# Performance work log

Measured on AMD Instinct MI355X. Metric: run time of the kernel, lower is better.

Reference implementation:

```python
import jax, jax.numpy as jnp
import numpy as np

EPS = 1e-8  # torch CosineSimilarity default eps


def setup_inputs() -> dict:
    key = jax.random.key(0)
    k1, k2, k3, k4 = jax.random.split(key, 4)
    cur_insts = jax.random.randint(k1, (200, 1024), 0, 50000)          # [S, B] token ids
    W = jax.random.normal(k2, (50000, 300), dtype=jnp.float32)          # embedding table
    train_embs = jax.random.normal(k3, (100000, 300), dtype=jnp.float32)  # pooled train embeddings
    y_train = jax.random.randint(k4, (100000,), 0, 1000)                # train labels
    return {"cur_insts": cur_insts, "W": W, "train_embs": train_embs, "y_train": y_train}


def reference(cur_insts, W, train_embs, y_train):
    # Embed + mean-pool over the sequence axis (dim 0 in the torch code)
    x = W[cur_insts].mean(axis=0)                                   # [B, d]
    # Cosine similarity: x.y / (max(||x||,eps) * max(||y||,eps))
    xn = jnp.maximum(jnp.linalg.norm(x, axis=1, keepdims=True), EPS)        # [B, 1]
    tn = jnp.maximum(jnp.linalg.norm(train_embs, axis=1, keepdims=True), EPS)  # [N, 1]
    sims = (x @ train_embs.T) / (xn * tn.T)                         # [B, N]
    nn_idx = jnp.argmax(sims, axis=1)                               # [B]
    scores = jnp.max(sims, axis=1)                                  # [B]
    y_pred = y_train[nn_idx]                                        # [B]
    return y_pred, scores
```

## Files before the change

### kernel.cpp

```cpp
#include <hip/hip_runtime.h>
#include <hip/hip_bf16.h>
#include <stdint.h>

#define EPS 1e-8f

typedef __attribute__((ext_vector_type(8))) short bf16x8;
typedef __attribute__((ext_vector_type(4))) float f32x4;
typedef unsigned long long u64;
typedef unsigned int u32;

constexpr int SEQ = 200;
constexpr int B_  = 1024;
constexpr int D_  = 300;
constexpr int DP  = 320;
constexpr int NT  = 100000;
constexpr int BM = 128, BN = 128, BK = 64;
constexpr int NSTRIP = 784;
constexpr int NTP = NSTRIP * BN;
constexpr int CAND_MAX = 4096;
#define MARGIN 2e-3f

__device__ __forceinline__ unsigned short f2bf(float f) {
    u32 b = __float_as_uint(f);
    return (unsigned short)((b + 0x7fffu + ((b >> 16) & 1u)) >> 16);
}
__device__ __forceinline__ u32 simkey(float s) {
    u32 b = __float_as_uint(s);
    return (b & 0x80000000u) ? ~b : (b | 0x80000000u);
}
__device__ __forceinline__ float keysim(u32 k) {
    u32 b = (k & 0x80000000u) ? (k & 0x7fffffffu) : ~k;
    return __uint_as_float(b);
}
__device__ __forceinline__ void gload_lds16(const void* g, void* l) {
    __builtin_amdgcn_global_load_lds(
        (const __attribute__((address_space(1))) unsigned int*)g,
        (__attribute__((address_space(3))) unsigned int*)l, 16, 0, 0);
}

__global__ __launch_bounds__(640) void pool_kernel(
    const int* __restrict__ ids, const float* __restrict__ W,
    float* __restrict__ x, unsigned short* __restrict__ xh,
    float* __restrict__ rxn)
{
    const int b = blockIdx.x;
    const int tid = threadIdx.x;
    __shared__ int sid[SEQ];
    __shared__ float part[640];
    for (int s = tid; s < SEQ; s += 640) sid[s] = ids[s * B_ + b];
    __syncthreads();
    const int half = (tid >= 320) ? 1 : 0;
    const int d = tid - half * 320;
    float a0 = 0.f, a1 = 0.f;
    if (d < D_) {
        const int s0 = half * (SEQ / 2);
        #pragma unroll 2
        for (int s = 0; s < SEQ / 2; s += 2) {
            a0 += W[(size_t)sid[s0 + s]     * D_ + d];
            a1 += W[(size_t)sid[s0 + s + 1] * D_ + d];
        }
    }
    part[tid] = a0 + a1;
    __syncthreads();
    float xv = 0.f;
    if (tid < 320) xv = (part[tid] + part[tid + 320]) * (1.0f / SEQ);
    __syncthreads();
    if (tid < 320) part[tid] = (tid < D_) ? xv * xv : 0.f;
    __syncthreads();
    if (tid < 64) {
        float s = 0.f;
        #pragma unroll
        for (int i = 0; i < 5; ++i) s += part[tid + i * 64];
        #pragma unroll
        for (int m = 32; m >= 1; m >>= 1) s += __shfl_xor(s, m, 64);
        if (tid == 0) rxn[b] = 1.0f / fmaxf(sqrtf(s), EPS);
    }
    if (tid < 320) {
        if (tid < D_) {
            x[(size_t)b * D_ + tid] = xv;
            xh[(size_t)b * DP + tid] = f2bf(xv);
        } else {
            xh[(size_t)b * DP + tid] = 0;
        }
    }
}

__global__ __launch_bounds__(256) void tnorm_kernel(
    const float* __restrict__ T, float* __restrict__ rtn,
    unsigned short* __restrict__ Tb)
{
    const int n = blockIdx.x * 4 + (threadIdx.x >> 6);
    const int lane = threadIdx.x & 63;
    if (n >= NTP) return;
    ushort4* tb = (ushort4*)(Tb + (size_t)n * DP);
    if (n >= NT) {
        ushort4 z = {0, 0, 0, 0};
        tb[lane] = z;
        if (lane < 16) tb[64 + lane] = z;
        return;
    }
    const float4* Tr = (const float4*)(T + (size_t)n * D_);
    float4 v = Tr[lane];
    float s = v.x * v.x + v.y * v.y + v.z * v.z + v.w * v.w;
    ushort4 o; o.x = f2bf(v.x); o.y = f2bf(v.y); o.z = f2bf(v.z); o.w = f2bf(v.w);
    tb[lane] = o;
    if (lane < 16) {
        if (lane < 11) {
            float4 w = Tr[64 + lane];
            s += w.x * w.x + w.y * w.y + w.z * w.z + w.w * w.w;
            ushort4 p; p.x = f2bf(w.x); p.y = f2bf(w.y); p.z = f2bf(w.z); p.w = f2bf(w.w);
            tb[64 + lane] = p;
        } else {
            ushort4 z = {0, 0, 0, 0};
            tb[64 + lane] = z;
        }
    }
    #pragma unroll
    for (int m = 32; m >= 1; m >>= 1) s += __shfl_xor(s, m, 64);
    if (lane == 0) rtn[n] = 1.0f / fmaxf(sqrtf(s), EPS);
}

__global__ __launch_bounds__(256, 3) void gemm_hh_kernel(
    const unsigned short* __restrict__ Ah, const unsigned short* __restrict__ Tb,
    const float* __restrict__ rxn, const float* __restrict__ rtn,
    u32* __restrict__ blockmax)
{
    __shared__ unsigned short sA[BM * BK];
    __shared__ unsigned short sB[BN * BK];
    __shared__ u32 sBest[BM];

    const int tid = threadIdx.x;
    const int g = blockIdx.x;
    const int k8 = g & 7;
    const int t = g >> 3;
    const int bMi = t & 7;
    const int strip = ((t >> 3) << 3) | k8;

    const int lane = tid & 63, wid = tid >> 6;
    const int wm = wid >> 1, wn = wid & 1;
    const int quad = lane >> 4, l15 = lane & 15;

    const unsigned short* pA[4];
    const unsigned short* pB[4];
    int ldsoff[4];
    #pragma unroll
    for (int j = 0; j < 4; ++j) {
        int L = (j * 4 + wid) * 64 + lane;
        int r = L >> 3;
        int c = (L & 7) ^ (r & 7);
        ldsoff[j] = (j * 4 + wid) * 1024;
        pA[j] = Ah + (size_t)(bMi * BM + r) * DP + c * 8;
        pB[j] = Tb + (size_t)(strip * BN + r) * DP + c * 8;
    }

    f32x4 acc[4][4] = {};

    for (int kp = 0; kp < DP; kp += BK) {
        #pragma unroll
        for (int j = 0; j < 4; ++j)
            gload_lds16(pA[j] + kp, (char*)sA + ldsoff[j]);
        #pragma unroll
        for (int j = 0; j < 4; ++j)
            gload_lds16(pB[j] + kp, (char*)sB + ldsoff[j]);
        __syncthreads();

        #pragma unroll
        for (int s = 0; s < 2; ++s) {
            bf16x8 fa[4], fb[4];
            #pragma unroll
            for (int f = 0; f < 4; ++f) {
                int ar = wm * 64 + f * 16 + l15;
                int ac = (s * 4 + quad) ^ (ar & 7);
                fa[f] = *(const bf16x8*)&sA[ar * BK + ac * 8];
                int br = wn * 64 + f * 16 + l15;
                int bc = (s * 4 + quad) ^ (br & 7);
                fb[f] = *(const bf16x8*)&sB[br * BK + bc * 8];
            }
            #pragma unroll
            for (int fm = 0; fm < 4; ++fm)
                #pragma unroll
                for (int fn = 0; fn < 4; ++fn)
                    acc[fm][fn] = __builtin_amdgcn_mfma_f32_16x16x32_bf16(
                        fa[fm], fb[fn], acc[fm][fn], 0, 0, 0);
        }
        __syncthreads();
    }

    if (tid < BM) sBest[tid] = 0u;
    __syncthreads();
    float rt[4];
    const int gn0 = strip * BN + wn * 64 + l15;
    #pragma unroll
    for (int fn = 0; fn < 4; ++fn)
        rt[fn] = (gn0 + fn * 16 < NT) ? rtn[gn0 + fn * 16] : 0.f;
    #pragma unroll
    for (int fm = 0; fm < 4; ++fm) {
        #pragma unroll
        for (int r = 0; r < 4; ++r) {
            int rowl = wm * 64 + fm * 16 + quad * 4 + r;
            float rx = rxn[bMi * BM + rowl];
            u32 bk = 0u;
            #pragma unroll
            for (int fn = 0; fn < 4; ++fn) {
                float sim = acc[fm][fn][r] * rx * rt[fn];
                u32 k = simkey(sim);
                bk = (k > bk) ? k : bk;
            }
            #pragma unroll
            for (int m = 1; m < 16; m <<= 1) {
                u32 o = __shfl_xor(bk, m, 64);
                bk = (o > bk) ? o : bk;
            }
            if (l15 == 0) atomicMax(&sBest[rowl], bk);
        }
    }
    __syncthreads();
    if (tid < BM)
        blockmax[(size_t)(bMi * BM + tid) * NSTRIP + strip] = sBest[tid];
}

__global__ __launch_bounds__(256) void scan_kernel(
    const u32* __restrict__ blockmax, u32* __restrict__ cand,
    u32* __restrict__ count)
{
    const int row = blockIdx.x;
    const int t = threadIdx.x;
    const u32* bmr = blockmax + (size_t)row * NSTRIP;
    u32 m = 0u;
    for (int j = t; j < NSTRIP; j += 256) { u32 e = bmr[j]; m = (e > m) ? e : m; }
    #pragma unroll
    for (int msk = 32; msk >= 1; msk >>= 1) {
        u32 o = __shfl_xor(m, msk, 64);
        m = (o > m) ? o : m;
    }
    __shared__ u32 wred[4];
    __shared__ float thr_s;
    if ((t & 63) == 0) wred[t >> 6] = m;
    __syncthreads();
    if (t == 0) {
        u32 gmx = wred[0];
        for (int i = 1; i < 4; ++i) gmx = (wred[i] > gmx) ? wred[i] : gmx;
        thr_s = keysim(gmx) - MARGIN;
    }
    __syncthreads();
    float thr = thr_s;
    for (int j = t; j < NSTRIP; j += 256) {
        if (keysim(bmr[j]) >= thr) {
            u32 p = atomicAdd(count, 1u);
            if (p < CAND_MAX) cand[p] = ((u32)row << 10) | (u32)j;
        }
    }
}

__global__ __launch_bounds__(256) void rescore_kernel(
    const u32* __restrict__ cand, const u32* __restrict__ count,
    const float* __restrict__ x, const float* __restrict__ T,
    const float* __restrict__ rxn, u64* __restrict__ winner)
{
    u32 cnt = *count; if (cnt > CAND_MAX) cnt = CAND_MAX;
    if (blockIdx.x >= cnt) return;
    u32 c = cand[blockIdx.x];
    const int row = c >> 10, strip = c & 1023;
    __shared__ float4 xs4[75];
    const int t = threadIdx.x;
    if (t < 75) xs4[t] = *(const float4*)&x[(size_t)row * D_ + t * 4];
    __syncthreads();
    const float rx = rxn[row];
    const int w = t >> 6, lane = t & 63;
    u64 best = 0ull;
    for (int cc = 0; cc < 32; ++cc) {
        int n = strip * BN + w * 32 + cc;
        if (n >= NT) break;
        const float4* Tr = (const float4*)(T + (size_t)n * D_);
        float4 v = Tr[lane], xv = xs4[lane];
        float dot = v.x * xv.x + v.y * xv.y + v.z * xv.z + v.w * xv.w;
        float tt  = v.x * v.x + v.y * v.y + v.z * v.z + v.w * v.w;
        if (lane < 11) {
            float4 v2 = Tr[lane + 64], x2 = xs4[lane + 64];
            dot += v2.x * x2.x + v2.y * x2.y + v2.z * x2.z + v2.w * x2.w;
            tt  += v2.x * v2.x + v2.y * v2.y + v2.z * v2.z + v2.w * v2.w;
        }
        #pragma unroll
        for (int m = 32; m >= 1; m >>= 1) {
            dot += __shfl_xor(dot, m, 64);
            tt  += __shfl_xor(tt, m, 64);
        }
        float sim = dot * rx / fmaxf(sqrtf(tt), EPS);
        u64 pk = ((u64)simkey(sim) << 32) | (u32)(~n);
        best = (pk > best) ? pk : best;
    }
    if (lane == 0 && best) atomicMax(&winner[row], best);
}

__global__ __launch_bounds__(64) void final_kernel(
    const u64* __restrict__ winner, const float* __restrict__ x,
    const float* __restrict__ T, const int* __restrict__ y_train,
    float* __restrict__ out)
{
    const int b = blockIdx.x;
    const int lane = threadIdx.x;
    int idx = (int)(~(u32)winner[b]);
    if (idx < 0 || idx >= NT) idx = 0;
    double dot = 0.0, nx = 0.0, nt = 0.0;
    for (int d = lane; d < D_; d += 64) {
        double xv = (double)x[(size_t)b * D_ + d];
        double tv = (double)T[(size_t)idx * D_ + d];
        dot += xv * tv; nx += xv * xv; nt += tv * tv;
    }
    #pragma unroll
    for (int m = 32; m >= 1; m >>= 1) {
        dot += __shfl_xor(dot, m, 64);
        nx  += __shfl_xor(nx, m, 64);
        nt  += __shfl_xor(nt, m, 64);
    }
    if (lane == 0) {
        double score = dot / (fmax(sqrt(nx), (double)EPS) * fmax(sqrt(nt), (double)EPS));
        out[b]      = (float)y_train[idx];
        out[B_ + b] = (float)score;
    }
}

extern "C" void kernel_launch(void* const* d_in, const int* in_sizes, int n_in,
                              void* d_out, int out_size, void* d_ws, size_t ws_size,
                              hipStream_t stream)
{
    const int*   ids = (const int*)d_in[0];
    const float* W   = (const float*)d_in[1];
    const float* T   = (const float*)d_in[2];
    const int*   y   = (const int*)d_in[3];

    char* ws = (char*)d_ws;
    size_t off = 0;
    float* x           = (float*)(ws + off);          off += (size_t)B_ * D_ * 4;
    unsigned short* xh = (unsigned short*)(ws + off); off += (size_t)B_ * DP * 2;
    float* rxn         = (float*)(ws + off);          off += (size_t)B_ * 4;
    float* rtn         = (float*)(ws + off);          off += (size_t)NT * 4;
    unsigned short* Tb = (unsigned short*)(ws + off); off += (size_t)NTP * DP * 2;
    u32* blockmax      = (u32*)(ws + off);            off += (size_t)B_ * NSTRIP * 4;
    u32* cand          = (u32*)(ws + off);            off += (size_t)CAND_MAX * 4;
    u64* winner        = (u64*)(ws + off);            off += (size_t)B_ * 8;
    u32* count         = (u32*)(ws + off);            off += 256;

    hipMemsetAsync(winner, 0, (size_t)B_ * 8 + 256, stream);
    pool_kernel<<<B_, 640, 0, stream>>>(ids, W, x, xh, rxn);
    tnorm_kernel<<<NTP / 4, 256, 0, stream>>>(T, rtn, Tb);
    gemm_hh_kernel<<<8 * NSTRIP, 256, 0, stream>>>(xh, Tb, rxn, rtn, blockmax);
    scan_kernel<<<B_, 256, 0, stream>>>(blockmax, cand, count);
    rescore_kernel<<<CAND_MAX, 256, 0, stream>>>(cand, count, x, T, rxn, winner);
    final_kernel<<<B_, 64, 0, stream>>>(winner, x, T, y, (float*)d_out);
}
```

Before: 397.6 us.

## Fuse pooling and table normalization, pre-normalize operands, parallelize rescoring

Merges the pooling and train-norm kernels into one launch and drops the memset by zeroing count and winner inside kernels. Both bf16 operands are pre-scaled by their reciprocal norms so the GEMM epilogue skips the per-element scaling and norm loads. The rescore kernel now spreads each candidate row over 4 lanes instead of a full wave, and CAND_MAX is doubled. Normalizing before bf16 rounding changes the rounding error, and the count reset in block 0 relies on stream ordering ahead of the scan kernel.

Result: faster. 373.6 us (-6.0%).

```diff
diff --git a/kernel.cpp b/kernel.cpp
--- a/kernel.cpp
+++ b/kernel.cpp
@@ -17,7 +17,9 @@
 constexpr int BM = 128, BN = 128, BK = 64;
 constexpr int NSTRIP = 784;
 constexpr int NTP = NSTRIP * BN;
-constexpr int CAND_MAX = 4096;
+constexpr int POOL_BLOCKS = B_;
+constexpr int TN_BLOCKS = (NTP + 9) / 10;
+constexpr int CAND_MAX = 8192;
 #define MARGIN 2e-3f
 
 __device__ __forceinline__ unsigned short f2bf(float f) {
@@ -38,91 +40,101 @@
         (__attribute__((address_space(3))) unsigned int*)l, 16, 0, 0);
 }
 
-__global__ __launch_bounds__(640) void pool_kernel(
+__global__ __launch_bounds__(640) void prep_kernel(
     const int* __restrict__ ids, const float* __restrict__ W,
+    const float* __restrict__ T,
     float* __restrict__ x, unsigned short* __restrict__ xh,
-    float* __restrict__ rxn)
-{
-    const int b = blockIdx.x;
+    float* __restrict__ rxn, unsigned short* __restrict__ Tb,
+    u32* __restrict__ count)
+{
     const int tid = threadIdx.x;
-    __shared__ int sid[SEQ];
-    __shared__ float part[640];
-    for (int s = tid; s < SEQ; s += 640) sid[s] = ids[s * B_ + b];
-    __syncthreads();
-    const int half = (tid >= 320) ? 1 : 0;
-    const int d = tid - half * 320;
-    float a0 = 0.f, a1 = 0.f;
-    if (d < D_) {
-        const int s0 = half * (SEQ / 2);
-        #pragma unroll 2
-        for (int s = 0; s < SEQ / 2; s += 2) {
-            a0 += W[(size_t)sid[s0 + s]     * D_ + d];
-            a1 += W[(size_t)sid[s0 + s + 1] * D_ + d];
-        }
-    }
-    part[tid] = a0 + a1;
-    __syncthreads();
-    float xv = 0.f;
-    if (tid < 320) xv = (part[tid] + part[tid + 320]) * (1.0f / SEQ);
-    __syncthreads();
-    if (tid < 320) part[tid] = (tid < D_) ? xv * xv : 0.f;
-    __syncthreads();
-    if (tid < 64) {
-        float s = 0.f;
-        #pragma unroll
-        for (int i = 0; i < 5; ++i) s += part[tid + i * 64];
+    if (blockIdx.x < POOL_BLOCKS) {
+        const int b = blockIdx.x;
+        if (b == 0 && tid == 0) *count = 0;
+        __shared__ int sid[SEQ];
+        __shared__ float part[640];
+        __shared__ float rns_s;
+        for (int s = tid; s < SEQ; s += 640) sid[s] = ids[s * B_ + b];
+        __syncthreads();
+        const int half = (tid >= 320) ? 1 : 0;
+        const int d = tid - half * 320;
+        float a0 = 0.f, a1 = 0.f;
+        if (d < D_) {
+            const int s0 = half * (SEQ / 2);
+            #pragma unroll 2
+            for (int s = 0; s < SEQ / 2; s += 2) {
+                a0 += W[(size_t)sid[s0 + s]     * D_ + d];
+                a1 += W[(size_t)sid[s0 + s + 1] * D_ + d];
+            }
+        }
+        part[tid] = a0 + a1;
+        __syncthreads();
+        float xv = 0.f;
+        if (tid < 320) xv = (part[tid] + part[tid + 320]) * (1.0f / SEQ);
+        __syncthreads();
+        if (tid < 320) part[tid] = (tid < D_) ? xv * xv : 0.f;
+        __syncthreads();
+        if (tid < 64) {
+            float s = 0.f;
+            #pragma unroll
+            for (int i = 0; i < 5; ++i) s += part[tid + i * 64];
+            #pragma unroll
+            for (int m = 32; m >= 1; m >>= 1) s += __shfl_xor(s, m, 64);
+            if (tid == 0) {
+                float r = 1.0f / fmaxf(sqrtf(s), EPS);
+                rxn[b] = r;
+                rns_s = r;
+            }
+        }
+        __syncthreads();
+        const float rns = rns_s;
+        if (tid < 320) {
+            if (tid < D_) {
+                x[(size_t)b * D_ + tid] = xv;
+                xh[(size_t)b * DP + tid] = f2bf(xv * rns);
+            } else {
+                xh[(size_t)b * DP + tid] = 0;
+            }
+        }
+    } else {
+        const int n = (blockIdx.x - POOL_BLOCKS) * 10 + (tid >> 6);
+        const int lane = tid & 63;
+        if (n >= NTP) return;
+        ushort4* tb = (ushort4*)(Tb + (size_t)n * DP);
+        if (n >= NT) {
+            ushort4 z = {0, 0, 0, 0};
+            tb[lane] = z;
+            if (lane < 16) tb[64 + lane] = z;
+            return;
+        }
+        const float4* Tr = (const float4*)(T + (size_t)n * D_);
+        float4 v = Tr[lane];
+        float s = v.x * v.x + v.y * v.y + v.z * v.z + v.w * v.w;
+        float4 w2 = make_float4(0.f, 0.f, 0.f, 0.f);
+        if (lane < 11) {
+            w2 = Tr[64 + lane];
+            s += w2.x * w2.x + w2.y * w2.y + w2.z * w2.z + w2.w * w2.w;
+        }
         #pragma unroll
         for (int m = 32; m >= 1; m >>= 1) s += __shfl_xor(s, m, 64);
-        if (tid == 0) rxn[b] = 1.0f / fmaxf(sqrtf(s), EPS);
-    }
-    if (tid < 320) {
-        if (tid < D_) {
-            x[(size_t)b * D_ + tid] = xv;
-            xh[(size_t)b * DP + tid] = f2bf(xv);
-        } else {
-            xh[(size_t)b * DP + tid] = 0;
-        }
-    }
-}
-
-__global__ __launch_bounds__(256) void tnorm_kernel(
-    const float* __restrict__ T, float* __restrict__ rtn,
-    unsigned short* __restrict__ Tb)
-{
-    const int n = blockIdx.x * 4 + (threadIdx.x >> 6);
-    const int lane = threadIdx.x & 63;
-    if (n >= NTP) return;
-    ushort4* tb = (ushort4*)(Tb + (size_t)n * DP);
-    if (n >= NT) {
-        ushort4 z = {0, 0, 0, 0};
-        tb[lane] = z;
-        if (lane < 16) tb[64 + lane] = z;
-        return;
-    }
-    const float4* Tr = (const float4*)(T + (size_t)n * D_);
-    float4 v = Tr[lane];
-    float s = v.x * v.x + v.y * v.y + v.z * v.z + v.w * v.w;
-    ushort4 o; o.x = f2bf(v.x); o.y = f2bf(v.y); o.z = f2bf(v.z); o.w = f2bf(v.w);
-    tb[lane] = o;
-    if (lane < 16) {
-        if (lane < 11) {
-            float4 w = Tr[64 + lane];
-            s += w.x * w.x + w.y * w.y + w.z * w.z + w.w * w.w;
-            ushort4 p; p.x = f2bf(w.x); p.y = f2bf(w.y); p.z = f2bf(w.z); p.w = f2bf(w.w);
+        const float rns = 1.0f / fmaxf(sqrtf(s), EPS);
+        ushort4 o;
+        o.x = f2bf(v.x * rns); o.y = f2bf(v.y * rns);
+        o.z = f2bf(v.z * rns); o.w = f2bf(v.w * rns);
+        tb[lane] = o;
+        if (lane < 16) {
+            ushort4 p = {0, 0, 0, 0};
+            if (lane < 11) {
+                p.x = f2bf(w2.x * rns); p.y = f2bf(w2.y * rns);
+                p.z = f2bf(w2.z * rns); p.w = f2bf(w2.w * rns);
+            }
             tb[64 + lane] = p;
-        } else {
-            ushort4 z = {0, 0, 0, 0};
-            tb[64 + lane] = z;
-        }
-    }
-    #pragma unroll
-    for (int m = 32; m >= 1; m >>= 1) s += __shfl_xor(s, m, 64);
-    if (lane == 0) rtn[n] = 1.0f / fmaxf(sqrtf(s), EPS);
+        }
+    }
 }
 
 __global__ __launch_bounds__(256, 3) void gemm_hh_kernel(
     const unsigned short* __restrict__ Ah, const unsigned short* __restrict__ Tb,
-    const float* __restrict__ rxn, const float* __restrict__ rtn,
     u32* __restrict__ blockmax)
 {
     __shared__ unsigned short sA[BM * BK];
@@ -188,22 +200,15 @@
 
     if (tid < BM) sBest[tid] = 0u;
     __syncthreads();
-    float rt[4];
-    const int gn0 = strip * BN + wn * 64 + l15;
-    #pragma unroll
-    for (int fn = 0; fn < 4; ++fn)
-        rt[fn] = (gn0 + fn * 16 < NT) ? rtn[gn0 + fn * 16] : 0.f;
     #pragma unroll
     for (int fm = 0; fm < 4; ++fm) {
         #pragma unroll
         for (int r = 0; r < 4; ++r) {
             int rowl = wm * 64 + fm * 16 + quad * 4 + r;
-            float rx = rxn[bMi * BM + rowl];
             u32 bk = 0u;
             #pragma unroll
             for (int fn = 0; fn < 4; ++fn) {
-                float sim = acc[fm][fn][r] * rx * rt[fn];
-                u32 k = simkey(sim);
+                u32 k = simkey(acc[fm][fn][r]);
                 bk = (k > bk) ? k : bk;
             }
             #pragma unroll
@@ -221,11 +226,16 @@
 
 __global__ __launch_bounds__(256) void scan_kernel(
     const u32* __restrict__ blockmax, u32* __restrict__ cand,
-    u32* __restrict__ count)
+    u32* __restrict__ count, u64* __restrict__ winner)
 {
     const int row = blockIdx.x;
     const int t = threadIdx.x;
+    const int w = t >> 6, lane = t & 63;
     const u32* bmr = blockmax + (size_t)row * NSTRIP;
+
+    __shared__ u32 wred[4];
+    __shared__ float thr_s;
+    if (t == 0) winner[row] = 0ull;
     u32 m = 0u;
     for (int j = t; j < NSTRIP; j += 256) { u32 e = bmr[j]; m = (e > m) ? e : m; }
     #pragma unroll
@@ -233,9 +243,7 @@
         u32 o = __shfl_xor(m, msk, 64);
         m = (o > m) ? o : m;
     }
-    __shared__ u32 wred[4];
-    __shared__ float thr_s;
-    if ((t & 63) == 0) wred[t >> 6] = m;
+    if (lane == 0) wred[w] = m;
     __syncthreads();
     if (t == 0) {
         u32 gmx = wred[0];
@@ -243,7 +251,7 @@
         thr_s = keysim(gmx) - MARGIN;
     }
     __syncthreads();
-    float thr = thr_s;
+    const float thr = thr_s;
     for (int j = t; j < NSTRIP; j += 256) {
         if (keysim(bmr[j]) >= thr) {
             u32 p = atomicAdd(count, 1u);
@@ -259,35 +267,44 @@
 {
     u32 cnt = *count; if (cnt > CAND_MAX) cnt = CAND_MAX;
     if (blockIdx.x >= cnt) return;
-    u32 c = cand[blockIdx.x];
+    const u32 c = cand[blockIdx.x];
     const int row = c >> 10, strip = c & 1023;
+
     __shared__ float4 xs4[75];
     const int t = threadIdx.x;
     if (t < 75) xs4[t] = *(const float4*)&x[(size_t)row * D_ + t * 4];
     __syncthreads();
+
     const float rx = rxn[row];
     const int w = t >> 6, lane = t & 63;
+    const int lane4 = lane & 3, colw = lane >> 2;
     u64 best = 0ull;
-    for (int cc = 0; cc < 32; ++cc) {
-        int n = strip * BN + w * 32 + cc;
-        if (n >= NT) break;
-        const float4* Tr = (const float4*)(T + (size_t)n * D_);
-        float4 v = Tr[lane], xv = xs4[lane];
-        float dot = v.x * xv.x + v.y * xv.y + v.z * xv.z + v.w * xv.w;
-        float tt  = v.x * v.x + v.y * v.y + v.z * v.z + v.w * v.w;
-        if (lane < 11) {
-            float4 v2 = Tr[lane + 64], x2 = xs4[lane + 64];
-            dot += v2.x * x2.x + v2.y * x2.y + v2.z * x2.z + v2.w * x2.w;
-            tt  += v2.x * v2.x + v2.y * v2.y + v2.z * v2.z + v2.w * v2.w;
-        }
-        #pragma unroll
-        for (int m = 32; m >= 1; m >>= 1) {
-            dot += __shfl_xor(dot, m, 64);
-            tt  += __shfl_xor(tt, m, 64);
-        }
-        float sim = dot * rx / fmaxf(sqrtf(tt), EPS);
-        u64 pk = ((u64)simkey(sim) << 32) | (u32)(~n);
-        best = (pk > best) ? pk : best;
+    #pragma unroll
+    for (int p = 0; p < 2; ++p) {
+        const int n = strip * BN + w * 32 + p * 16 + colw;
+        if (n < NT) {
+            const float4* Tr = (const float4*)(T + (size_t)n * D_);
+            float dot = 0.f, tt = 0.f;
+            #pragma unroll
+            for (int jj = 0; jj < 19; ++jj) {
+                int idx = lane4 + jj * 4;
+                if (idx < 75) {
+                    float4 v = Tr[idx], xv = xs4[idx];
+                    dot += v.x * xv.x + v.y * xv.y + v.z * xv.z + v.w * xv.w;
+                    tt  += v.x * v.x + v.y * v.y + v.z * v.z + v.w * v.w;
+                }
+            }
+            dot += __shfl_xor(dot, 1, 64); tt += __shfl_xor(tt, 1, 64);
+            dot += __shfl_xor(dot, 2, 64); tt += __shfl_xor(tt, 2, 64);
+            float sim = dot * rx / fmaxf(sqrtf(tt), EPS);
+            u64 pk = ((u64)simkey(sim) << 32) | (u32)(~n);
+            best = (pk > best) ? pk : best;
+        }
+    }
+    #pragma unroll
+    for (int m = 1; m < 64; m <<= 1) {
+        u64 o = __shfl_xor(best, m, 64);
+        best = (o > best) ? o : best;
     }
     if (lane == 0 && best) atomicMax(&winner[row], best);
 }
@@ -334,18 +351,15 @@
     float* x           = (float*)(ws + off);          off += (size_t)B_ * D_ * 4;
     unsigned short* xh = (unsigned short*)(ws + off); off += (size_t)B_ * DP * 2;
     float* rxn         = (float*)(ws + off);          off += (size_t)B_ * 4;
-    float* rtn         = (float*)(ws + off);          off += (size_t)NT * 4;
     unsigned short* Tb = (unsigned short*)(ws + off); off += (size_t)NTP * DP * 2;
     u32* blockmax      = (u32*)(ws + off);            off += (size_t)B_ * NSTRIP * 4;
     u32* cand          = (u32*)(ws + off);            off += (size_t)CAND_MAX * 4;
     u64* winner        = (u64*)(ws + off);            off += (size_t)B_ * 8;
     u32* count         = (u32*)(ws + off);            off += 256;
 
-    hipMemsetAsync(winner, 0, (size_t)B_ * 8 + 256, stream);
-    pool_kernel<<<B_, 640, 0, stream>>>(ids, W, x, xh, rxn);
-    tnorm_kernel<<<NTP / 4, 256, 0, stream>>>(T, rtn, Tb);
-    gemm_hh_kernel<<<8 * NSTRIP, 256, 0, stream>>>(xh, Tb, rxn, rtn, blockmax);
-    scan_kernel<<<B_, 256, 0, stream>>>(blockmax, cand, count);
+    prep_kernel<<<POOL_BLOCKS + TN_BLOCKS, 640, 0, stream>>>(ids, W, T, x, xh, rxn, Tb, count);
+    gemm_hh_kernel<<<NSTRIP * 8, 256, 0, stream>>>(xh, Tb, blockmax);
+    scan_kernel<<<B_, 256, 0, stream>>>(blockmax, cand, count, winner);
     rescore_kernel<<<CAND_MAX, 256, 0, stream>>>(cand, count, x, T, rxn, winner);
     final_kernel<<<B_, 64, 0, stream>>>(winner, x, T, y, (float*)d_out);
 }
```
